# Optimization experiments

Hardware: AMD Instinct MI355X
Metric: run time of the kernel (lower is better)

Reference implementation:

```python
import jax, jax.numpy as jnp
import numpy as np
import math

B, M, N, K = 4, 8192, 8192, 16
FD = 64       # in_fdim == out_fdim (residual add)
HID = 128     # args.hidden_dim
G = 8         # args.ngroups


def index_points(points, idx):
    # points: (B, C, N), idx: (B, M, K) -> (B, C, M, K)
    return jax.vmap(lambda p, i: p[:, i])(points, idx)


def conv1d(x, w, b):  # 1x1 Conv1d: x (B,Ci,M), w (Co,Ci)
    return jnp.einsum('oi,bim->bom', w, x) + b[None, :, None]


def conv2d(x, w, b):  # 1x1 Conv2d: x (B,Ci,M,K), w (Co,Ci)
    return jnp.einsum('oi,bimk->bomk', w, x) + b[None, :, None, None]


def group_norm(x, w, b, eps=1e-5):
    # torch GroupNorm over (C//G, M, K) per group per sample
    Bb, C, Mm, Kk = x.shape
    xr = x.reshape(Bb, G, C // G, Mm, Kk)
    mu = xr.mean(axis=(2, 3, 4), keepdims=True)
    var = xr.var(axis=(2, 3, 4), keepdims=True)
    xr = (xr - mu) * jax.lax.rsqrt(var + eps)
    return xr.reshape(Bb, C, Mm, Kk) * w[None, :, None, None] + b[None, :, None, None]


def setup_inputs() -> dict:
    key = jax.random.key(0)
    ks = jax.random.split(key, 24)
    s = 0.05
    inp = {
        'q_xyzs': jax.random.normal(ks[0], (B, 3, M), jnp.float32),
        'k_xyzs': jax.random.normal(ks[1], (B, 3, N), jnp.float32),
        'q_feats': jax.random.normal(ks[2], (B, FD, M), jnp.float32),
        'k_feats': jax.random.normal(ks[3], (B, FD, N), jnp.float32),
        'v_feats': jax.random.normal(ks[4], (B, FD, N), jnp.float32),
        'knn_idx': jax.random.randint(ks[5], (B, M, K), 0, N),
        'mask': jnp.ones((B, M, K), dtype=bool),
        'wq_w': jax.random.normal(ks[6], (HID, FD)) * s, 'wq_b': jnp.zeros((HID,)),
        'wk_w': jax.random.normal(ks[7], (HID, FD)) * s, 'wk_b': jnp.zeros((HID,)),
        'wv_w': jax.random.normal(ks[8], (HID, FD)) * s, 'wv_b': jnp.zeros((HID,)),
        'd1_w': jax.random.normal(ks[9], (HID, 3)) * s, 'd1_b': jnp.zeros((HID,)),
        'dgn_w': jnp.ones((HID,)), 'dgn_b': jnp.zeros((HID,)),
        'd2_w': jax.random.normal(ks[10], (HID, HID)) * s, 'd2_b': jnp.zeros((HID,)),
        'g1_w': jax.random.normal(ks[11], (HID, HID)) * s, 'g1_b': jnp.zeros((HID,)),
        'ggn_w': jnp.ones((HID,)), 'ggn_b': jnp.zeros((HID,)),
        'g2_w': jax.random.normal(ks[12], (HID, HID)) * s, 'g2_b': jnp.zeros((HID,)),
        'post_w': jax.random.normal(ks[13], (FD, HID)) * s, 'post_b': jnp.zeros((FD,)),
    }
    return inp


def reference(q_xyzs, k_xyzs, q_feats, k_feats, v_feats, knn_idx, mask,
              wq_w, wq_b, wk_w, wk_b, wv_w, wv_b,
              d1_w, d1_b, dgn_w, dgn_b, d2_w, d2_b,
              g1_w, g1_b, ggn_w, ggn_b, g2_w, g2_b,
              post_w, post_b):
    knn_xyzs = index_points(k_xyzs, knn_idx)                 # (B,3,M,K)
    pre = q_feats
    query = conv1d(q_feats, wq_w, wq_b)                      # (B,HID,M)
    key = index_points(conv1d(k_feats, wk_w, wk_b), knn_idx) # (B,HID,M,K)
    value = index_points(conv1d(v_feats, wv_w, wv_b), knn_idx)

    rel = q_xyzs[:, :, :, None] - knn_xyzs                   # (B,3,M,K)
    pos_enc = conv2d(jax.nn.relu(group_norm(conv2d(rel, d1_w, d1_b), dgn_w, dgn_b)), d2_w, d2_b)

    attn_in = query[:, :, :, None] - key + pos_enc
    attn = conv2d(jax.nn.relu(group_norm(conv2d(attn_in, g1_w, g1_b), ggn_w, ggn_b)), g2_w, g2_b)
    attn = attn / math.sqrt(HID)
    attn = jnp.where(mask[:, None], attn, -jnp.finfo(attn.dtype).max)
    attn = jax.nn.softmax(attn, axis=-1)                     # over neighbor axis K

    res = jnp.einsum('bcmk,bcmk->bcm', attn, value + pos_enc)
    return conv1d(res, post_w, post_b) + pre
```

## Files before the change

### kernel.cpp

```cpp
#include <hip/hip_runtime.h>
#include <hip/hip_bf16.h>

typedef __attribute__((ext_vector_type(8))) short short8;
typedef __attribute__((ext_vector_type(4))) float f32x4;
typedef unsigned short ushort_t;

#define B_    4
#define M_    8192
#define N_    8192
#define KNN   16
#define FD    64
#define HID   128
#define CNT   (M_*KNN)
#define SCALE 0.08838834764831845f

#define QT_OFF       0ULL
#define KT_OFF       4194304ULL
#define VT_OFF       6291456ULL
#define WD2_OFF      8388608ULL
#define WFO_OFF      8396800ULL
#define WG2_OFF      8404992ULL
#define WQ2T_OFF     8413184ULL
#define WK2T_OFF     8421376ULL
#define WVT_OFF      8429568ULL
#define POSTT_OFF    8437760ULL
#define G2BS_OFF     8445952ULL
#define BQ_OFF       8446080ULL
#define BK_OFF       8446208ULL
#define HAFF_OFF     8446336ULL
#define RELSTATS_OFF 8448384ULL
#define YSUM_OFF     8448448ULL
#define YSQ_OFF      8448960ULL
#define GGNA_OFF     8449472ULL
#define GGNB_OFF     8449984ULL
#define OUTS_OFF     8450496ULL
#define YW_OFF       10547648ULL
#define VPW_OFF      44102080ULL
#define WS_END_FULL  77656512ULL
#define WS_NEED_FULL (WS_END_FULL * 4ULL)
#define WS_NEED_YW   ((YW_OFF + 33554432ULL) * 4ULL)

__device__ __forceinline__ ushort_t f2bf(float x) {
    return (ushort_t)((__float_as_uint(x) + 0x8000u) >> 16);
}
__device__ __forceinline__ unsigned pk2bf(float a, float b) {
    unsigned ua = __float_as_uint(a) + 0x8000u;
    unsigned ub = __float_as_uint(b) + 0x8000u;
    return (ua >> 16) | (ub & 0xFFFF0000u);
}
__device__ __forceinline__ float bf2f(ushort_t b) {
    union { unsigned u; float f; } v; v.u = ((unsigned)b) << 16;
    return v.f;
}

__global__ __launch_bounds__(256) void k_prep(
    const float* __restrict__ d2, const float* __restrict__ g1, const float* __restrict__ g2,
    const float* __restrict__ wq, const float* __restrict__ wk, const float* __restrict__ wv,
    const float* __restrict__ post, const float* __restrict__ g2b,
    const float* __restrict__ wq_b, const float* __restrict__ wk_b,
    const float* __restrict__ d2b, const float* __restrict__ g1b,
    float* __restrict__ ws)
{
    int tid = blockIdx.x * 256 + threadIdx.x;
    if (tid < 16384) {
        int j = tid & 7, lane = (tid >> 3) & 63, s = (tid >> 9) & 3, ct = tid >> 11;
        int row = ct*16 + (lane & 15);
        int colk = s*32 + (lane >> 4)*8 + j;
        ((ushort_t*)(ws + WD2_OFF))[tid] = f2bf(d2[row*HID + colk]);
        ((ushort_t*)(ws + WG2_OFF))[tid] = f2bf(g2[row*HID + colk] * SCALE);
        float acc = 0.f;
        #pragma unroll 8
        for (int t = 0; t < HID; t++) acc += g1[row*HID + t] * d2[t*HID + colk];
        ((ushort_t*)(ws + WFO_OFF))[tid] = f2bf(acc);
    }
    if (tid < 8192) {
        int f = tid >> 7, j = tid & 127;
        ws[POSTT_OFF + j*64 + f] = post[tid];
        int i = tid >> 7, c = tid & 127;
        float aq = 0.f, ak = 0.f;
        #pragma unroll 8
        for (int h = 0; h < HID; h++) {
            float g = g1[c*HID + h];
            aq += g * wq[h*FD + i];
            ak += g * wk[h*FD + i];
        }
        ws[WQ2T_OFF + tid] = aq;
        ws[WK2T_OFF + tid] = ak;
        ws[WVT_OFF + tid] = wv[c*FD + i];
    }
    if (tid < 128) {
        ws[G2BS_OFF + tid] = g2b[tid] * SCALE;
        float bq = g1b[tid], bk = 0.f;
        #pragma unroll 8
        for (int h = 0; h < HID; h++) {
            float g = g1[tid*HID + h];
            bq += g * (wq_b[h] + d2b[h]);
            bk += g * wk_b[h];
        }
        ws[BQ_OFF + tid] = bq;
        ws[BK_OFF + tid] = bk;
    }
}

__global__ __launch_bounds__(256) void k_transform(
    const float* __restrict__ qf, const float* __restrict__ kf, const float* __restrict__ vf,
    const float* __restrict__ wv_b, float* __restrict__ ws)
{
    __shared__ __align__(16) float sF[64*36];
    int tid = threadIdx.x;
    int t = blockIdx.y;
    int gm0 = blockIdx.x * 32;
    int b = gm0 >> 13, m0 = gm0 & (M_-1);
    const float* in = (t==0) ? qf : (t==1) ? kf : vf;
    const float* wT = ws + ((t==0) ? WQ2T_OFF : (t==1) ? WK2T_OFF : WVT_OFF);
    {
        int i = tid >> 2, sg = tid & 3;
        const float* src = in + ((size_t)b*FD + i)*M_ + m0 + sg*8;
        *(f32x4*)&sF[i*36 + sg*8]     = *(const f32x4*)src;
        *(f32x4*)&sF[i*36 + sg*8 + 4] = *(const f32x4*)(src + 4);
    }
    __syncthreads();
    int c = tid & 127, h = tid >> 7;
    float bc = (t==0) ? ws[BQ_OFF + c] : (t==1) ? ws[BK_OFF + c] : wv_b[c];
    float acc[16];
    #pragma unroll
    for (int p = 0; p < 16; p++) acc[p] = bc;
    #pragma unroll 4
    for (int i = 0; i < 64; i++) {
        float w = wT[i*128 + c];
        #pragma unroll
        for (int pq = 0; pq < 4; pq++) {
            f32x4 fv = *(const f32x4*)&sF[i*36 + h*16 + pq*4];
            acc[pq*4+0] += w*fv[0]; acc[pq*4+1] += w*fv[1];
            acc[pq*4+2] += w*fv[2]; acc[pq*4+3] += w*fv[3];
        }
    }
    if (t == 0) {
        #pragma unroll
        for (int p = 0; p < 16; p++)
            ws[QT_OFF + (size_t)(gm0 + h*16 + p)*HID + c] = acc[p];
    } else {
        ushort_t* o = (ushort_t*)(ws + ((t==1) ? KT_OFF : VT_OFF));
        #pragma unroll
        for (int p = 0; p < 16; p++)
            o[(size_t)(gm0 + h*16 + p)*HID + c] = f2bf(acc[p]);
    }
}

__global__ __launch_bounds__(256) void k_relstats(
    const float* __restrict__ qx, const float* __restrict__ kx,
    const int* __restrict__ knn, float* __restrict__ ws)
{
    int tid = threadIdx.x;
    int b = blockIdx.y;
    int m = blockIdx.x * 256 + tid;
    const float* qb = qx + (size_t)b*3*M_;
    const float* kb = kx + (size_t)b*3*N_;
    const int* kn = knn + ((size_t)b*M_ + m)*KNN;
    float a[9] = {0,0,0,0,0,0,0,0,0};
    float q0 = qb[m], q1 = qb[M_+m], q2 = qb[2*M_+m];
    #pragma unroll
    for (int k = 0; k < KNN; k++) {
        int id = kn[k];
        float r0 = q0 - kb[id], r1 = q1 - kb[N_+id], r2 = q2 - kb[2*N_+id];
        a[0]+=r0; a[1]+=r1; a[2]+=r2;
        a[3]+=r0*r0; a[4]+=r0*r1; a[5]+=r0*r2;
        a[6]+=r1*r1; a[7]+=r1*r2; a[8]+=r2*r2;
    }
    __shared__ float red[4];
    float* rs = ws + RELSTATS_OFF + b*16;
    for (int q = 0; q < 9; q++) {
        float v = a[q];
        #pragma unroll
        for (int o = 32; o > 0; o >>= 1) v += __shfl_down(v, o, 64);
        if ((tid & 63) == 0) red[tid >> 6] = v;
        __syncthreads();
        if (tid == 0) atomicAdd(&rs[q], red[0]+red[1]+red[2]+red[3]);
        __syncthreads();
    }
}

__global__ __launch_bounds__(512) void k_dgn(
    const float* __restrict__ d1w, const float* __restrict__ d1b,
    const float* __restrict__ gw, const float* __restrict__ gb,
    float* __restrict__ ws)
{
    __shared__ float sm_[512], sq_[512], smu[32], srs[32];
    int t = threadIdx.x, b = t >> 7, c = t & 127;
    const float* rs = ws + RELSTATS_OFF + b*16;
    float inv = 1.0f / (float)CNT;
    float x0 = rs[0]*inv, x1 = rs[1]*inv, x2 = rs[2]*inv;
    float S00 = rs[3]*inv, S01 = rs[4]*inv, S02 = rs[5]*inv;
    float S11 = rs[6]*inv, S12 = rs[7]*inv, S22 = rs[8]*inv;
    float w0 = d1w[c*3], w1 = d1w[c*3+1], w2 = d1w[c*3+2], bc = d1b[c];
    float mc = w0*x0 + w1*x1 + w2*x2 + bc;
    float qc = w0*w0*S00 + w1*w1*S11 + w2*w2*S22
             + 2.f*(w0*w1*S01 + w0*w2*S02 + w1*w2*S12)
             + 2.f*bc*(mc - bc) + bc*bc;
    sm_[t] = mc; sq_[t] = qc;
    __syncthreads();
    if (t < 32) {
        int bb = t >> 3, g = t & 7;
        float mu = 0, ey = 0;
        for (int j = 0; j < 16; j++) { mu += sm_[bb*128 + g*16 + j]; ey += sq_[bb*128 + g*16 + j]; }
        mu *= (1.f/16.f); ey *= (1.f/16.f);
        smu[t] = mu; srs[t] = rsqrtf(ey - mu*mu + 1e-5f);
    }
    __syncthreads();
    int g = c >> 4;
    float al = gw[c] * srs[b*8 + g];
    float be = gb[c] - smu[b*8 + g] * al;
    f32x4 h; h[0] = al*w0; h[1] = al*w1; h[2] = al*w2; h[3] = al*bc + be;
    *(f32x4*)(ws + HAFF_OFF + ((size_t)b*128 + c)*4) = h;
}

__global__ __launch_bounds__(512) void k_ggn(
    const float* __restrict__ gw, const float* __restrict__ gb, float* __restrict__ ws)
{
    __shared__ float smu[32], srs[32];
    int t = threadIdx.x, b = t >> 7, c = t & 127;
    if (t < 32) {
        int bb = t >> 3, g = t & 7;
        float s1 = 0, s2 = 0;
        for (int j = 0; j < 16; j++) {
            s1 += ws[YSUM_OFF + bb*128 + g*16 + j];
            s2 += ws[YSQ_OFF  + bb*128 + g*16 + j];
        }
        float invn = 1.f / (16.f * (float)CNT);
        float mu = s1*invn, ey = s2*invn;
        smu[t] = mu; srs[t] = rsqrtf(ey - mu*mu + 1e-5f);
    }
    __syncthreads();
    int g = c >> 4;
    float al = gw[c] * srs[b*8 + g];
    float be = gb[c] - smu[b*8 + g] * al;
    ws[GGNA_OFF + b*128 + c] = al;
    ws[GGNB_OFF + b*128 + c] = be;
}

struct SmemStats {
    f32x4 haff[128];
    float rel[4][16][4];
    ushort_t tH[4][16*136];
    float ga[128], gb[128];
    int idx[64];
};

__global__ __launch_bounds__(256, 4) void k_statsbig(
    const float* __restrict__ qx, const float* __restrict__ kx, const int* __restrict__ knn,
    const float* __restrict__ d2b, float* __restrict__ ws)
{
    __shared__ SmemStats sm;
    int tid = threadIdx.x, wid = tid >> 6, lane = tid & 63;
    int ln = lane & 15, q = lane >> 4;
    int gm0 = blockIdx.x * 4;
    int b = gm0 >> 13, m0 = gm0 & (M_-1);
    int ct0 = wid * 2;

    if (tid < 64) {
        int id = knn[(size_t)gm0*KNN + tid];
        sm.idx[tid] = id;
        int p = tid >> 4, nn = tid & 15;
        int m = m0 + p;
        sm.rel[p][nn][0] = qx[(size_t)b*3*M_ + m]        - kx[(size_t)b*3*N_ + id];
        sm.rel[p][nn][1] = qx[(size_t)b*3*M_ + M_ + m]   - kx[(size_t)b*3*N_ + N_ + id];
        sm.rel[p][nn][2] = qx[(size_t)b*3*M_ + 2*M_ + m] - kx[(size_t)b*3*N_ + 2*N_ + id];
    }
    if (tid < 128) {
        sm.haff[tid] = *(const f32x4*)(ws + HAFF_OFF + ((size_t)b*128 + tid)*4);
        sm.ga[tid] = 0.f; sm.gb[tid] = 0.f;
    }
    __syncthreads();

    const ushort_t* ktb = (const ushort_t*)(ws + KT_OFF);
    const ushort_t* vtb = (const ushort_t*)(ws + VT_OFF);

    uint2 kvp[4][2], vvp[4][2];
    #pragma unroll
    for (int p = 0; p < 4; p++) {
        int id = sm.idx[p*16 + ln];
        const ushort_t* kr = ktb + ((size_t)b*N_ + id)*HID;
        const ushort_t* vr = vtb + ((size_t)b*N_ + id)*HID;
        #pragma unroll
        for (int cc = 0; cc < 2; cc++) {
            kvp[p][cc] = *(const uint2*)(kr + (ct0+cc)*16 + q*4);
            vvp[p][cc] = *(const uint2*)(vr + (ct0+cc)*16 + q*4);
        }
    }

    {
        int p = tid >> 6, n = (tid >> 2) & 15, cb = tid & 3;
        float r0 = sm.rel[p][n][0];
        float r1 = sm.rel[p][n][1];
        float r2 = sm.rel[p][n][2];
        unsigned* dst = (unsigned*)&sm.tH[p][n*136 + cb*32];
        int rot = ((((n >> 3) & 1) | (((cb >> 1) & 1) << 1)) << 2);
        #pragma unroll
        for (int t = 0; t < 16; t++) {
            int o = (t + rot) & 15;
            f32x4 h1 = sm.haff[cb*32 + 2*o];
            f32x4 h2 = sm.haff[cb*32 + 2*o + 1];
            float a = fmaf(h1[0], r0, fmaf(h1[1], r1, fmaf(h1[2], r2, h1[3])));
            float c = fmaf(h2[0], r0, fmaf(h2[1], r1, fmaf(h2[2], r2, h2[3])));
            dst[o] = pk2bf(a > 0.f ? a : 0.f, c > 0.f ? c : 0.f);
        }
    }
    __syncthreads();

    const short8* wfo = (const short8*)(ws + WFO_OFF);
    const short8* wd2 = (const short8*)(ws + WD2_OFF);
    uint2* yw8 = (uint2*)(ws + YW_OFF);
    uint2* vp8 = (uint2*)(ws + VPW_OFF);

    float s1[2][4], s2[2][4];
    #pragma unroll
    for (int cc = 0; cc < 2; cc++)
        #pragma unroll
        for (int r = 0; r < 4; r++) { s1[cc][r] = 0.f; s2[cc][r] = 0.f; }

    #pragma unroll
    for (int p = 0; p < 4; p++) {
        int gm = gm0 + p;
        short8 bh[4];
        #pragma unroll
        for (int s = 0; s < 4; s++)
            bh[s] = *(const short8*)&sm.tH[p][ln*136 + s*32 + q*8];

        #pragma unroll
        for (int cc = 0; cc < 2; cc++) {
            f32x4 a = {0.f,0.f,0.f,0.f};
            #pragma unroll
            for (int s = 0; s < 4; s++)
                a = __builtin_amdgcn_mfma_f32_16x16x32_bf16(wd2[((ct0+cc)*4+s)*64 + lane], bh[s], a, 0,0,0);
            int row0 = (ct0+cc)*16 + q*4;
            f32x4 bi = *(const f32x4*)(d2b + row0);
            uint2 vv = vvp[p][cc];
            uint2 pv;
            pv.x = pk2bf(a[0]+bi[0]+bf2f((ushort_t)(vv.x & 0xffff)),
                         a[1]+bi[1]+bf2f((ushort_t)(vv.x >> 16)));
            pv.y = pk2bf(a[2]+bi[2]+bf2f((ushort_t)(vv.y & 0xffff)),
                         a[3]+bi[3]+bf2f((ushort_t)(vv.y >> 16)));
            vp8[((size_t)gm*8 + ct0+cc)*64 + lane] = pv;
        }
        #pragma unroll
        for (int cc = 0; cc < 2; cc++) {
            f32x4 a = {0.f,0.f,0.f,0.f};
            #pragma unroll
            for (int s = 0; s < 4; s++)
                a = __builtin_amdgcn_mfma_f32_16x16x32_bf16(wfo[((ct0+cc)*4+s)*64 + lane], bh[s], a, 0,0,0);
            int row0 = (ct0+cc)*16 + q*4;
            f32x4 qv = *(const f32x4*)(ws + QT_OFF + (size_t)gm*HID + row0);
            uint2 kv = kvp[p][cc];
            float y0 = a[0] + qv[0] - bf2f((ushort_t)(kv.x & 0xffff));
            float y1 = a[1] + qv[1] - bf2f((ushort_t)(kv.x >> 16));
            float y2 = a[2] + qv[2] - bf2f((ushort_t)(kv.y & 0xffff));
            float y3 = a[3] + qv[3] - bf2f((ushort_t)(kv.y >> 16));
            s1[cc][0]+=y0; s1[cc][1]+=y1; s1[cc][2]+=y2; s1[cc][3]+=y3;
            s2[cc][0]+=y0*y0; s2[cc][1]+=y1*y1; s2[cc][2]+=y2*y2; s2[cc][3]+=y3*y3;
            uint2 yv; yv.x = pk2bf(y0,y1); yv.y = pk2bf(y2,y3);
            yw8[((size_t)gm*8 + ct0+cc)*64 + lane] = yv;
        }
    }

    #pragma unroll
    for (int cc = 0; cc < 2; cc++)
        #pragma unroll
        for (int r = 0; r < 4; r++) {
            float v1 = s1[cc][r], v2 = s2[cc][r];
            v1 += __shfl_xor(v1,1,64); v1 += __shfl_xor(v1,2,64);
            v1 += __shfl_xor(v1,4,64); v1 += __shfl_xor(v1,8,64);
            v2 += __shfl_xor(v2,1,64); v2 += __shfl_xor(v2,2,64);
            v2 += __shfl_xor(v2,4,64); v2 += __shfl_xor(v2,8,64);
            if (ln == 0) {
                atomicAdd(&sm.ga[(ct0+cc)*16 + q*4 + r], v1);
                atomicAdd(&sm.gb[(ct0+cc)*16 + q*4 + r], v2);
            }
        }
    __syncthreads();
    if (tid < 128) {
        atomicAdd(&ws[YSUM_OFF + b*128 + tid], sm.ga[tid]);
        atomicAdd(&ws[YSQ_OFF  + b*128 + tid], sm.gb[tid]);
    }
}

struct SmemFinal {
    ushort_t tY[4][16*136];
    ushort_t tVP[4][16*136];
    float ga[128], gb[128];
    float res[4][128];
};

__global__ __launch_bounds__(256, 4) void k_final(
    const float* __restrict__ postb, float* __restrict__ ws)
{
    __shared__ SmemFinal sm;
    int tid = threadIdx.x, wid = tid >> 6, lane = tid & 63;
    int ln = lane & 15, q = lane >> 4;
    int gm0 = blockIdx.x * 4;
    int b = gm0 >> 13;
    int ct0 = wid * 2;

    if (tid < 128) {
        sm.ga[tid] = ws[GGNA_OFF + b*128 + tid];
        sm.gb[tid] = ws[GGNB_OFF + b*128 + tid];
    }
    __syncthreads();

    const uint2* yw8 = (const uint2*)(ws + YW_OFF);
    const uint2* vp8 = (const uint2*)(ws + VPW_OFF);

    #pragma unroll
    for (int p = 0; p < 4; p++) {
        int gm = gm0 + p;
        #pragma unroll
        for (int cc = 0; cc < 2; cc++) {
            int ct = ct0 + cc, row0 = ct*16 + q*4;
            uint2 yv = yw8[((size_t)gm*8 + ct)*64 + lane];
            f32x4 ga = *(const f32x4*)&sm.ga[row0];
            f32x4 gb = *(const f32x4*)&sm.gb[row0];
            float t0 = fmaf(ga[0], bf2f((ushort_t)(yv.x & 0xffff)), gb[0]);
            float t1 = fmaf(ga[1], bf2f((ushort_t)(yv.x >> 16)),    gb[1]);
            float t2 = fmaf(ga[2], bf2f((ushort_t)(yv.y & 0xffff)), gb[2]);
            float t3 = fmaf(ga[3], bf2f((ushort_t)(yv.y >> 16)),    gb[3]);
            uint2 yq2;
            yq2.x = pk2bf(t0 > 0.f ? t0 : 0.f, t1 > 0.f ? t1 : 0.f);
            yq2.y = pk2bf(t2 > 0.f ? t2 : 0.f, t3 > 0.f ? t3 : 0.f);
            *(uint2*)&sm.tY[p][ln*136 + row0] = yq2;
            *(uint2*)&sm.tVP[p][ln*136 + row0] = vp8[((size_t)gm*8 + ct)*64 + lane];
        }
    }
    __syncthreads();

    {
        const short8* wg2 = (const short8*)(ws + WG2_OFF);
        #pragma unroll
        for (int p = 0; p < 4; p++) {
            short8 ay[4];
            #pragma unroll
            for (int s = 0; s < 4; s++)
                ay[s] = *(const short8*)&sm.tY[p][ln*136 + s*32 + q*8];
            #pragma unroll
            for (int cc = 0; cc < 2; cc++) {
                int cout = (ct0+cc)*16 + ln;
                f32x4 a = {0.f,0.f,0.f,0.f};
                #pragma unroll
                for (int s = 0; s < 4; s++)
                    a = __builtin_amdgcn_mfma_f32_16x16x32_bf16(ay[s], wg2[((ct0+cc)*4+s)*64 + lane], a, 0,0,0);
                float zb = ws[G2BS_OFF + cout];
                float den = 0.f, num = 0.f;
                #pragma unroll
                for (int r = 0; r < 4; r++) {
                    float e = __expf(a[r] + zb);
                    den += e;
                    num += e * bf2f(sm.tVP[p][(q*4+r)*136 + cout]);
                }
                den += __shfl_xor(den, 16, 64); den += __shfl_xor(den, 32, 64);
                num += __shfl_xor(num, 16, 64); num += __shfl_xor(num, 32, 64);
                if (q == 0) sm.res[p][cout] = num / den;
            }
        }
    }
    __syncthreads();

    {
        int f = tid >> 2, p = tid & 3;
        const float* pt = ws + POSTT_OFF;
        const float* rr = sm.res[p];
        float acc = postb[f];
        #pragma unroll 8
        for (int j = 0; j < 128; j++) acc += pt[j*64 + f] * rr[j];
        ws[OUTS_OFF + (size_t)(gm0 + p)*FD + f] = acc;
    }
}

struct SmemPipe {
    union {
        ushort_t tP[4][16*136];
        struct { f32x4 haff[128]; float rel[4][16][4]; } pre;
    } u;
    ushort_t tH[4][16*136];
    float ga[128], gb[128];
    float res[4][128];
    int idx[64];
};

template<bool STATS, bool STOREY, bool LOADY>
__global__ __launch_bounds__(256, 4) void k_pipe(
    const float* __restrict__ qx, const float* __restrict__ kx, const int* __restrict__ knn,
    const float* __restrict__ d2b, const float* __restrict__ postb,
    float* __restrict__ ws)
{
    __shared__ SmemPipe sm;
    int tid = threadIdx.x, wid = tid >> 6, lane = tid & 63;
    int ln = lane & 15, q = lane >> 4;
    int gm0 = blockIdx.x * 4;
    int b = gm0 >> 13, m0 = gm0 & (M_-1);
    int ct0 = wid * 2;

    if (tid < 64) {
        int id = knn[(size_t)gm0*KNN + tid];
        sm.idx[tid] = id;
        int p = tid >> 4, nn = tid & 15;
        int m = m0 + p;
        sm.u.pre.rel[p][nn][0] = qx[(size_t)b*3*M_ + m]        - kx[(size_t)b*3*N_ + id];
        sm.u.pre.rel[p][nn][1] = qx[(size_t)b*3*M_ + M_ + m]   - kx[(size_t)b*3*N_ + N_ + id];
        sm.u.pre.rel[p][nn][2] = qx[(size_t)b*3*M_ + 2*M_ + m] - kx[(size_t)b*3*N_ + 2*N_ + id];
    }
    if (tid < 128) {
        sm.u.pre.haff[tid] = *(const f32x4*)(ws + HAFF_OFF + ((size_t)b*128 + tid)*4);
        if (STATS) { sm.ga[tid] = 0.f; sm.gb[tid] = 0.f; }
        else { sm.ga[tid] = ws[GGNA_OFF + b*128 + tid]; sm.gb[tid] = ws[GGNB_OFF + b*128 + tid]; }
    }
    __syncthreads();

    const ushort_t* ktb = (const ushort_t*)(ws + KT_OFF);
    const ushort_t* vtb = (const ushort_t*)(ws + VT_OFF);

    uint2 kvp[4][2];
    if (!LOADY) {
        #pragma unroll
        for (int p = 0; p < 4; p++) {
            int id = sm.idx[p*16 + ln];
            const ushort_t* kr = ktb + ((size_t)b*N_ + id)*HID;
            #pragma unroll
            for (int cc = 0; cc < 2; cc++)
                kvp[p][cc] = *(const uint2*)(kr + (ct0+cc)*16 + q*4);
        }
    }

    {
        int p = tid >> 6, n = (tid >> 2) & 15, cb = tid & 3;
        float r0 = sm.u.pre.rel[p][n][0];
        float r1 = sm.u.pre.rel[p][n][1];
        float r2 = sm.u.pre.rel[p][n][2];
        unsigned* dst = (unsigned*)&sm.tH[p][n*136 + cb*32];
        int rot = ((((n >> 3) & 1) | (((cb >> 1) & 1) << 1)) << 2);
        #pragma unroll
        for (int t = 0; t < 16; t++) {
            int o = (t + rot) & 15;
            f32x4 h1 = sm.u.pre.haff[cb*32 + 2*o];
            f32x4 h2 = sm.u.pre.haff[cb*32 + 2*o + 1];
            float a = fmaf(h1[0], r0, fmaf(h1[1], r1, fmaf(h1[2], r2, h1[3])));
            float c = fmaf(h2[0], r0, fmaf(h2[1], r1, fmaf(h2[2], r2, h2[3])));
            dst[o] = pk2bf(a > 0.f ? a : 0.f, c > 0.f ? c : 0.f);
        }
    }
    __syncthreads();

    const short8* wfo = (const short8*)(ws + WFO_OFF);
    const short8* wd2 = (const short8*)(ws + WD2_OFF);

    float s1[2][4], s2[2][4];
    if (STATS) {
        #pragma unroll
        for (int cc = 0; cc < 2; cc++)
            #pragma unroll
            for (int r = 0; r < 4; r++) { s1[cc][r] = 0.f; s2[cc][r] = 0.f; }
    }
    uint2 yp[4][2];
    f32x4 bid2[2], ga_[2], gb_[2];
    #pragma unroll
    for (int cc = 0; cc < 2; cc++) {
        int row0 = (ct0+cc)*16 + q*4;
        if (!STATS) {
            bid2[cc] = *(const f32x4*)(d2b + row0);
            ga_[cc] = *(const f32x4*)&sm.ga[row0];
            gb_[cc] = *(const f32x4*)&sm.gb[row0];
        }
    }

    #pragma unroll
    for (int p = 0; p < 4; p++) {
        int gm = gm0 + p;
        short8 bh[4];
        #pragma unroll
        for (int s = 0; s < 4; s++)
            bh[s] = *(const short8*)&sm.tH[p][ln*136 + s*32 + q*8];

        if (!LOADY) {
            #pragma unroll
            for (int cc = 0; cc < 2; cc++) {
                int row0 = (ct0+cc)*16 + q*4;
                f32x4 a = {0.f,0.f,0.f,0.f};
                #pragma unroll
                for (int s = 0; s < 4; s++)
                    a = __builtin_amdgcn_mfma_f32_16x16x32_bf16(wfo[((ct0+cc)*4+s)*64 + lane], bh[s], a, 0,0,0);
                f32x4 qv = *(const f32x4*)(ws + QT_OFF + (size_t)gm*HID + row0);
                uint2 kv = kvp[p][cc];
                float y0 = a[0] + qv[0] - bf2f((ushort_t)(kv.x & 0xffff));
                float y1 = a[1] + qv[1] - bf2f((ushort_t)(kv.x >> 16));
                float y2 = a[2] + qv[2] - bf2f((ushort_t)(kv.y & 0xffff));
                float y3 = a[3] + qv[3] - bf2f((ushort_t)(kv.y >> 16));
                if (STATS) {
                    s1[cc][0]+=y0; s1[cc][1]+=y1; s1[cc][2]+=y2; s1[cc][3]+=y3;
                    s2[cc][0]+=y0*y0; s2[cc][1]+=y1*y1; s2[cc][2]+=y2*y2; s2[cc][3]+=y3*y3;
                    if (STOREY) { yp[p][cc].x = pk2bf(y0,y1); yp[p][cc].y = pk2bf(y2,y3); }
                } else {
                    float t0 = fmaf(ga_[cc][0], y0, gb_[cc][0]);
                    float t1 = fmaf(ga_[cc][1], y1, gb_[cc][1]);
                    float t2 = fmaf(ga_[cc][2], y2, gb_[cc][2]);
                    float t3 = fmaf(ga_[cc][3], y3, gb_[cc][3]);
                    yp[p][cc].x = pk2bf(t0 > 0.f ? t0 : 0.f, t1 > 0.f ? t1 : 0.f);
                    yp[p][cc].y = pk2bf(t2 > 0.f ? t2 : 0.f, t3 > 0.f ? t3 : 0.f);
                }
            }
        }
        if (!STATS) {
            #pragma unroll
            for (int cc = 0; cc < 2; cc++) {
                f32x4 a = {0.f,0.f,0.f,0.f};
                #pragma unroll
                for (int s = 0; s < 4; s++)
                    a = __builtin_amdgcn_mfma_f32_16x16x32_bf16(wd2[((ct0+cc)*4+s)*64 + lane], bh[s], a, 0,0,0);
                int row0 = (ct0+cc)*16 + q*4;
                uint2 pv;
                pv.x = pk2bf(a[0]+bid2[cc][0], a[1]+bid2[cc][1]);
                pv.y = pk2bf(a[2]+bid2[cc][2], a[3]+bid2[cc][3]);
                *(uint2*)&sm.u.tP[p][ln*136 + row0] = pv;
            }
        }
    }

    if (STATS) {
        if (STOREY) {
            __syncthreads();
            #pragma unroll
            for (int p = 0; p < 4; p++)
                #pragma unroll
                for (int cc = 0; cc < 2; cc++)
                    *(uint2*)&sm.tH[p][ln*136 + (ct0+cc)*16 + q*4] = yp[p][cc];
            __syncthreads();
            {
                int p = tid >> 6, n = (tid >> 2) & 15, cb = tid & 3;
                ushort_t* yw = (ushort_t*)(ws + YW_OFF);
                const short8* src = (const short8*)&sm.tH[p][n*136 + cb*32];
                short8* dst = (short8*)(yw + ((size_t)(gm0+p)*16 + n)*HID + cb*32);
                #pragma unroll
                for (int u = 0; u < 4; u++) dst[u] = src[u];
            }
        }
        #pragma unroll
        for (int cc = 0; cc < 2; cc++)
            #pragma unroll
            for (int r = 0; r < 4; r++) {
                float v1 = s1[cc][r], v2 = s2[cc][r];
                v1 += __shfl_xor(v1,1,64); v1 += __shfl_xor(v1,2,64);
                v1 += __shfl_xor(v1,4,64); v1 += __shfl_xor(v1,8,64);
                v2 += __shfl_xor(v2,1,64); v2 += __shfl_xor(v2,2,64);
                v2 += __shfl_xor(v2,4,64); v2 += __shfl_xor(v2,8,64);
                if (ln == 0) {
                    atomicAdd(&sm.ga[(ct0+cc)*16 + q*4 + r], v1);
                    atomicAdd(&sm.gb[(ct0+cc)*16 + q*4 + r], v2);
                }
            }
        __syncthreads();
        if (tid < 128) {
            atomicAdd(&ws[YSUM_OFF + b*128 + tid], sm.ga[tid]);
            atomicAdd(&ws[YSQ_OFF  + b*128 + tid], sm.gb[tid]);
        }
        return;
    }

    __syncthreads();

    if (LOADY) {
        int p = tid >> 6, n = (tid >> 2) & 15, cb = tid & 3;
        const ushort_t* yw = (const ushort_t*)(ws + YW_OFF);
        const short8* src = (const short8*)(yw + ((size_t)(gm0+p)*16 + n)*HID + cb*32);
        ushort_t* dst = &sm.tH[p][n*136 + cb*32];
        #pragma unroll
        for (int u = 0; u < 4; u++) {
            short8 yv8 = src[u];
            unsigned w[4];
            #pragma unroll
            for (int j = 0; j < 4; j++) {
                float ga0 = sm.ga[cb*32 + u*8 + j*2],   gb0 = sm.gb[cb*32 + u*8 + j*2];
                float ga1 = sm.ga[cb*32 + u*8 + j*2+1], gb1 = sm.gb[cb*32 + u*8 + j*2+1];
                float ya = fmaf(ga0, bf2f((ushort_t)yv8[j*2]),   gb0);
                float yb = fmaf(ga1, bf2f((ushort_t)yv8[j*2+1]), gb1);
                w[j] = pk2bf(ya > 0.f ? ya : 0.f, yb > 0.f ? yb : 0.f);
            }
            *(short8*)(dst + u*8) = *(short8*)w;
        }
    } else {
        #pragma unroll
        for (int p = 0; p < 4; p++)
            #pragma unroll
            for (int cc = 0; cc < 2; cc++)
                *(uint2*)&sm.tH[p][ln*136 + (ct0+cc)*16 + q*4] = yp[p][cc];
    }
    {
        int p = tid >> 6, n = (tid >> 2) & 15, cb = tid & 3;
        int id = sm.idx[p*16 + n];
        const ushort_t* vr = vtb + ((size_t)b*N_ + id)*HID + cb*32;
        ushort_t* pr = &sm.u.tP[p][n*136 + cb*32];
        #pragma unroll
        for (int u = 0; u < 4; u++) {
            short8 vv = *(const short8*)(vr + u*8);
            short8 pp = *(const short8*)(pr + u*8);
            unsigned w[4];
            #pragma unroll
            for (int j = 0; j < 4; j++) {
                float a = bf2f((ushort_t)vv[j*2])   + bf2f((ushort_t)pp[j*2]);
                float c = bf2f((ushort_t)vv[j*2+1]) + bf2f((ushort_t)pp[j*2+1]);
                w[j] = pk2bf(a, c);
            }
            *(short8*)(pr + u*8) = *(short8*)w;
        }
    }
    __syncthreads();

    {
        const short8* wg2 = (const short8*)(ws + WG2_OFF);
        #pragma unroll
        for (int p = 0; p < 4; p++) {
            short8 ay[4];
            #pragma unroll
            for (int s = 0; s < 4; s++)
                ay[s] = *(const short8*)&sm.tH[p][ln*136 + s*32 + q*8];
            #pragma unroll
            for (int cc = 0; cc < 2; cc++) {
                int cout = (ct0+cc)*16 + ln;
                f32x4 a = {0.f,0.f,0.f,0.f};
                #pragma unroll
                for (int s = 0; s < 4; s++)
                    a = __builtin_amdgcn_mfma_f32_16x16x32_bf16(ay[s], wg2[((ct0+cc)*4+s)*64 + lane], a, 0,0,0);
                float zb = ws[G2BS_OFF + cout];
                float den = 0.f, num = 0.f;
                #pragma unroll
                for (int r = 0; r < 4; r++) {
                    float e = __expf(a[r] + zb);
                    den += e;
                    num += e * bf2f(sm.u.tP[p][(q*4+r)*136 + cout]);
                }
                den += __shfl_xor(den, 16, 64); den += __shfl_xor(den, 32, 64);
                num += __shfl_xor(num, 16, 64); num += __shfl_xor(num, 32, 64);
                if (q == 0) sm.res[p][cout] = num / den;
            }
        }
    }
    __syncthreads();

    {
        int f = tid >> 2, p = tid & 3;
        const float* pt = ws + POSTT_OFF;
        const float* rr = sm.res[p];
        float acc = postb[f];
        #pragma unroll 8
        for (int j = 0; j < 128; j++) acc += pt[j*64 + f] * rr[j];
        ws[OUTS_OFF + (size_t)(gm0 + p)*FD + f] = acc;
    }
}

__global__ __launch_bounds__(256) void k_out(
    const float* __restrict__ qf, const float* __restrict__ ws, float* __restrict__ out)
{
    __shared__ float sT[64][65];
    int tid = threadIdx.x;
    int b = blockIdx.y, m0 = blockIdx.x * 64;
    const float* stg = ws + OUTS_OFF + ((size_t)b*M_ + m0)*FD;
    #pragma unroll
    for (int it = 0; it < 16; it++) {
        int idx = it*256 + tid;
        sT[idx >> 6][idx & 63] = stg[idx];
    }
    __syncthreads();
    #pragma unroll
    for (int it = 0; it < 16; it++) {
        int idx = it*256 + tid;
        int f = idx >> 6, mm = idx & 63;
        size_t o = (size_t)b*FD*M_ + (size_t)f*M_ + m0 + mm;
        out[o] = sT[mm][f] + qf[o];
    }
}

extern "C" void kernel_launch(void* const* d_in, const int* in_sizes, int n_in,
                              void* d_out, int out_size, void* d_ws, size_t ws_size,
                              hipStream_t stream)
{
    const float* q_xyzs = (const float*)d_in[0];
    const float* k_xyzs = (const float*)d_in[1];
    const float* q_feats= (const float*)d_in[2];
    const float* k_feats= (const float*)d_in[3];
    const float* v_feats= (const float*)d_in[4];
    const int*   knn    = (const int*)d_in[5];
    const float* wq_w = (const float*)d_in[7];  const float* wq_b = (const float*)d_in[8];
    const float* wk_w = (const float*)d_in[9];  const float* wk_b = (const float*)d_in[10];
    const float* wv_w = (const float*)d_in[11]; const float* wv_b = (const float*)d_in[12];
    const float* d1_w = (const float*)d_in[13]; const float* d1_b = (const float*)d_in[14];
    const float* dgn_w= (const float*)d_in[15]; const float* dgn_b= (const float*)d_in[16];
    const float* d2_w = (const float*)d_in[17]; const float* d2_b = (const float*)d_in[18];
    const float* g1_w = (const float*)d_in[19]; const float* g1_b = (const float*)d_in[20];
    const float* ggn_w= (const float*)d_in[21]; const float* ggn_b= (const float*)d_in[22];
    const float* g2_w = (const float*)d_in[23]; const float* g2_b = (const float*)d_in[24];
    const float* post_w=(const float*)d_in[25]; const float* post_b=(const float*)d_in[26];
    float* ws  = (float*)d_ws;
    float* out = (float*)d_out;

    bool full = (ws_size >= WS_NEED_FULL);
    bool yw   = (ws_size >= WS_NEED_YW);

    hipMemsetAsync(ws + RELSTATS_OFF, 0, 1088*sizeof(float), stream);

    k_prep<<<64, 256, 0, stream>>>(d2_w, g1_w, g2_w, wq_w, wk_w, wv_w,
                                   post_w, g2_b, wq_b, wk_b, d2_b, g1_b, ws);
    k_transform<<<dim3(B_*M_/32, 3), 256, 0, stream>>>(q_feats, k_feats, v_feats, wv_b, ws);
    k_relstats<<<dim3(M_/256, B_), 256, 0, stream>>>(q_xyzs, k_xyzs, knn, ws);
    k_dgn<<<1, 512, 0, stream>>>(d1_w, d1_b, dgn_w, dgn_b, ws);
    if (full) {
        k_statsbig<<<B_*M_/4, 256, 0, stream>>>(q_xyzs, k_xyzs, knn, d2_b, ws);
        k_ggn<<<1, 512, 0, stream>>>(ggn_w, ggn_b, ws);
        k_final<<<B_*M_/4, 256, 0, stream>>>(post_b, ws);
    } else if (yw) {
        k_pipe<true, true, false><<<B_*M_/4, 256, 0, stream>>>(q_xyzs, k_xyzs, knn, d2_b, post_b, ws);
        k_ggn<<<1, 512, 0, stream>>>(ggn_w, ggn_b, ws);
        k_pipe<false, false, true><<<B_*M_/4, 256, 0, stream>>>(q_xyzs, k_xyzs, knn, d2_b, post_b, ws);
    } else {
        k_pipe<true, false, false><<<B_*M_/4, 256, 0, stream>>>(q_xyzs, k_xyzs, knn, d2_b, post_b, ws);
        k_ggn<<<1, 512, 0, stream>>>(ggn_w, ggn_b, ws);
        k_pipe<false, false, false><<<B_*M_/4, 256, 0, stream>>>(q_xyzs, k_xyzs, knn, d2_b, post_b, ws);
    }
    k_out<<<dim3(M_/64, B_), 256, 0, stream>>>(q_feats, ws, out);
}
```

Measured before the change: 489.6 us.

## Store pre-norm activations as fp8, Q as bf16, fuse output residual into final kernels

The pre-GroupNorm activation buffer is now written as packed fp8 instead of bf16, and the query projection is stored as bf16 instead of fp32. This halves the intermediate traffic and shrinks the workspace. The separate k_out transpose kernel is removed, and the final kernels write the residual-added output straight to the output tensor. The Y layout in k_pipe is switched to the lane-native fragment order, and Y/VP loads are prefetched into registers early. Fp8 quantisation of pre-norm values adds precision risk, and the direct output stores are strided by M, which may be poorly coalesced.

```diff
diff --git a/kernel.cpp b/kernel.cpp
--- a/kernel.cpp
+++ b/kernel.cpp
@@ -3,6 +3,7 @@
 
 typedef __attribute__((ext_vector_type(8))) short short8;
 typedef __attribute__((ext_vector_type(4))) float f32x4;
+typedef __attribute__((ext_vector_type(2))) float f32x2;
 typedef unsigned short ushort_t;
 
 #define B_    4
@@ -15,29 +16,27 @@
 #define SCALE 0.08838834764831845f
 
 #define QT_OFF       0ULL
-#define KT_OFF       4194304ULL
-#define VT_OFF       6291456ULL
-#define WD2_OFF      8388608ULL
-#define WFO_OFF      8396800ULL
-#define WG2_OFF      8404992ULL
-#define WQ2T_OFF     8413184ULL
-#define WK2T_OFF     8421376ULL
-#define WVT_OFF      8429568ULL
-#define POSTT_OFF    8437760ULL
-#define G2BS_OFF     8445952ULL
-#define BQ_OFF       8446080ULL
-#define BK_OFF       8446208ULL
-#define HAFF_OFF     8446336ULL
-#define RELSTATS_OFF 8448384ULL
-#define YSUM_OFF     8448448ULL
-#define YSQ_OFF      8448960ULL
-#define GGNA_OFF     8449472ULL
-#define GGNB_OFF     8449984ULL
-#define OUTS_OFF     8450496ULL
-#define YW_OFF       10547648ULL
-#define VPW_OFF      44102080ULL
-#define WS_END_FULL  77656512ULL
-#define WS_NEED_FULL (WS_END_FULL * 4ULL)
+#define KT_OFF       2097152ULL
+#define VT_OFF       4194304ULL
+#define WD2_OFF      6291456ULL
+#define WFO_OFF      6299648ULL
+#define WG2_OFF      6307840ULL
+#define WQ2T_OFF     6316032ULL
+#define WK2T_OFF     6324224ULL
+#define WVT_OFF      6332416ULL
+#define POSTT_OFF    6340608ULL
+#define G2BS_OFF     6348800ULL
+#define BQ_OFF       6348928ULL
+#define BK_OFF       6349056ULL
+#define HAFF_OFF     6349184ULL
+#define RELSTATS_OFF 6351232ULL
+#define YSUM_OFF     6351296ULL
+#define YSQ_OFF      6351808ULL
+#define GGNA_OFF     6352320ULL
+#define GGNB_OFF     6352832ULL
+#define YW_OFF       6353344ULL
+#define VPW_OFF      23130560ULL
+#define WS_NEED_F8   (56684992ULL * 4ULL)
 #define WS_NEED_YW   ((YW_OFF + 33554432ULL) * 4ULL)
 
 __device__ __forceinline__ ushort_t f2bf(float x) {
@@ -51,6 +50,11 @@
 __device__ __forceinline__ float bf2f(ushort_t b) {
     union { unsigned u; float f; } v; v.u = ((unsigned)b) << 16;
     return v.f;
+}
+__device__ __forceinline__ unsigned pk4fp8(float a, float b, float c, float d) {
+    int v = __builtin_amdgcn_cvt_pk_fp8_f32(a, b, 0, false);
+    v = __builtin_amdgcn_cvt_pk_fp8_f32(c, d, v, true);
+    return (unsigned)v;
 }
 
 __global__ __launch_bounds__(256) void k_prep(
@@ -135,16 +139,10 @@
             acc[pq*4+2] += w*fv[2]; acc[pq*4+3] += w*fv[3];
         }
     }
-    if (t == 0) {
-        #pragma unroll
-        for (int p = 0; p < 16; p++)
-            ws[QT_OFF + (size_t)(gm0 + h*16 + p)*HID + c] = acc[p];
-    } else {
-        ushort_t* o = (ushort_t*)(ws + ((t==1) ? KT_OFF : VT_OFF));
-        #pragma unroll
-        for (int p = 0; p < 16; p++)
-            o[(size_t)(gm0 + h*16 + p)*HID + c] = f2bf(acc[p]);
-    }
+    ushort_t* o = (ushort_t*)(ws + ((t==0) ? QT_OFF : (t==1) ? KT_OFF : VT_OFF));
+    #pragma unroll
+    for (int p = 0; p < 16; p++)
+        o[(size_t)(gm0 + h*16 + p)*HID + c] = f2bf(acc[p]);
 }
 
 __global__ __launch_bounds__(256) void k_relstats(
@@ -272,6 +270,7 @@
     }
     __syncthreads();
 
+    const ushort_t* qtb = (const ushort_t*)(ws + QT_OFF);
     const ushort_t* ktb = (const ushort_t*)(ws + KT_OFF);
     const ushort_t* vtb = (const ushort_t*)(ws + VT_OFF);
 
@@ -309,7 +308,7 @@
 
     const short8* wfo = (const short8*)(ws + WFO_OFF);
     const short8* wd2 = (const short8*)(ws + WD2_OFF);
-    uint2* yw8 = (uint2*)(ws + YW_OFF);
+    unsigned* yf8 = (unsigned*)(ws + YW_OFF);
     uint2* vp8 = (uint2*)(ws + VPW_OFF);
 
     float s1[2][4], s2[2][4];
@@ -349,16 +348,15 @@
             for (int s = 0; s < 4; s++)
                 a = __builtin_amdgcn_mfma_f32_16x16x32_bf16(wfo[((ct0+cc)*4+s)*64 + lane], bh[s], a, 0,0,0);
             int row0 = (ct0+cc)*16 + q*4;
-            f32x4 qv = *(const f32x4*)(ws + QT_OFF + (size_t)gm*HID + row0);
+            uint2 qv = *(const uint2*)(qtb + (size_t)gm*HID + row0);
             uint2 kv = kvp[p][cc];
-            float y0 = a[0] + qv[0] - bf2f((ushort_t)(kv.x & 0xffff));
-            float y1 = a[1] + qv[1] - bf2f((ushort_t)(kv.x >> 16));
-            float y2 = a[2] + qv[2] - bf2f((ushort_t)(kv.y & 0xffff));
-            float y3 = a[3] + qv[3] - bf2f((ushort_t)(kv.y >> 16));
+            float y0 = a[0] + bf2f((ushort_t)(qv.x & 0xffff)) - bf2f((ushort_t)(kv.x & 0xffff));
+            float y1 = a[1] + bf2f((ushort_t)(qv.x >> 16))    - bf2f((ushort_t)(kv.x >> 16));
+            float y2 = a[2] + bf2f((ushort_t)(qv.y & 0xffff)) - bf2f((ushort_t)(kv.y & 0xffff));
+            float y3 = a[3] + bf2f((ushort_t)(qv.y >> 16))    - bf2f((ushort_t)(kv.y >> 16));
             s1[cc][0]+=y0; s1[cc][1]+=y1; s1[cc][2]+=y2; s1[cc][3]+=y3;
             s2[cc][0]+=y0*y0; s2[cc][1]+=y1*y1; s2[cc][2]+=y2*y2; s2[cc][3]+=y3*y3;
-            uint2 yv; yv.x = pk2bf(y0,y1); yv.y = pk2bf(y2,y3);
-            yw8[((size_t)gm*8 + ct0+cc)*64 + lane] = yv;
+            yf8[((size_t)gm*8 + ct0+cc)*64 + lane] = pk4fp8(y0, y1, y2, y3);
         }
     }
 
@@ -391,14 +389,26 @@
 };
 
 __global__ __launch_bounds__(256, 4) void k_final(
-    const float* __restrict__ postb, float* __restrict__ ws)
+    const float* __restrict__ postb, const float* __restrict__ qf,
+    float* __restrict__ ws, float* __restrict__ out)
 {
     __shared__ SmemFinal sm;
     int tid = threadIdx.x, wid = tid >> 6, lane = tid & 63;
     int ln = lane & 15, q = lane >> 4;
     int gm0 = blockIdx.x * 4;
-    int b = gm0 >> 13;
+    int b = gm0 >> 13, m0 = gm0 & (M_-1);
     int ct0 = wid * 2;
+
+    const unsigned* yf8 = (const unsigned*)(ws + YW_OFF);
+    const uint2* vp8 = (const uint2*)(ws + VPW_OFF);
+    unsigned yv_[4][2]; uint2 vp_[4][2];
+    #pragma unroll
+    for (int p = 0; p < 4; p++)
+        #pragma unroll
+        for (int cc = 0; cc < 2; cc++) {
+            yv_[p][cc] = yf8[((size_t)(gm0+p)*8 + ct0+cc)*64 + lane];
+            vp_[p][cc] = vp8[((size_t)(gm0+p)*8 + ct0+cc)*64 + lane];
+        }
 
     if (tid < 128) {
         sm.ga[tid] = ws[GGNA_OFF + b*128 + tid];
@@ -406,29 +416,25 @@
     }
     __syncthreads();
 
-    const uint2* yw8 = (const uint2*)(ws + YW_OFF);
-    const uint2* vp8 = (const uint2*)(ws + VPW_OFF);
-
-    #pragma unroll
-    for (int p = 0; p < 4; p++) {
-        int gm = gm0 + p;
+    #pragma unroll
+    for (int p = 0; p < 4; p++)
         #pragma unroll
         for (int cc = 0; cc < 2; cc++) {
-            int ct = ct0 + cc, row0 = ct*16 + q*4;
-            uint2 yv = yw8[((size_t)gm*8 + ct)*64 + lane];
+            int row0 = (ct0+cc)*16 + q*4;
+            f32x2 lo = __builtin_amdgcn_cvt_pk_f32_fp8((int)yv_[p][cc], false);
+            f32x2 hi = __builtin_amdgcn_cvt_pk_f32_fp8((int)yv_[p][cc], true);
             f32x4 ga = *(const f32x4*)&sm.ga[row0];
             f32x4 gb = *(const f32x4*)&sm.gb[row0];
-            float t0 = fmaf(ga[0], bf2f((ushort_t)(yv.x & 0xffff)), gb[0]);
-            float t1 = fmaf(ga[1], bf2f((ushort_t)(yv.x >> 16)),    gb[1]);
-            float t2 = fmaf(ga[2], bf2f((ushort_t)(yv.y & 0xffff)), gb[2]);
-            float t3 = fmaf(ga[3], bf2f((ushort_t)(yv.y >> 16)),    gb[3]);
+            float t0 = fmaf(ga[0], lo[0], gb[0]);
+            float t1 = fmaf(ga[1], lo[1], gb[1]);
+            float t2 = fmaf(ga[2], hi[0], gb[2]);
+            float t3 = fmaf(ga[3], hi[1], gb[3]);
             uint2 yq2;
             yq2.x = pk2bf(t0 > 0.f ? t0 : 0.f, t1 > 0.f ? t1 : 0.f);
             yq2.y = pk2bf(t2 > 0.f ? t2 : 0.f, t3 > 0.f ? t3 : 0.f);
             *(uint2*)&sm.tY[p][ln*136 + row0] = yq2;
-            *(uint2*)&sm.tVP[p][ln*136 + row0] = vp8[((size_t)gm*8 + ct)*64 + lane];
-        }
-    }
+            *(uint2*)&sm.tVP[p][ln*136 + row0] = vp_[p][cc];
+        }
     __syncthreads();
 
     {
@@ -469,7 +475,8 @@
         float acc = postb[f];
         #pragma unroll 8
         for (int j = 0; j < 128; j++) acc += pt[j*64 + f] * rr[j];
-        ws[OUTS_OFF + (size_t)(gm0 + p)*FD + f] = acc;
+        size_t o = (size_t)b*FD*M_ + (size_t)f*M_ + m0 + p;
+        out[o] = acc + qf[o];
     }
 }
 
@@ -488,7 +495,7 @@
 __global__ __launch_bounds__(256, 4) void k_pipe(
     const float* __restrict__ qx, const float* __restrict__ kx, const int* __restrict__ knn,
     const float* __restrict__ d2b, const float* __restrict__ postb,
-    float* __restrict__ ws)
+    const float* __restrict__ qf, float* __restrict__ ws, float* __restrict__ out)
 {
     __shared__ SmemPipe sm;
     int tid = threadIdx.x, wid = tid >> 6, lane = tid & 63;
@@ -496,6 +503,16 @@
     int gm0 = blockIdx.x * 4;
     int b = gm0 >> 13, m0 = gm0 & (M_-1);
     int ct0 = wid * 2;
+
+    uint2 ywp[4][2];
+    if (LOADY) {
+        const uint2* yw8 = (const uint2*)(ws + YW_OFF);
+        #pragma unroll
+        for (int p = 0; p < 4; p++)
+            #pragma unroll
+            for (int cc = 0; cc < 2; cc++)
+                ywp[p][cc] = yw8[((size_t)(gm0+p)*8 + ct0+cc)*64 + lane];
+    }
 
     if (tid < 64) {
         int id = knn[(size_t)gm0*KNN + tid];
@@ -513,6 +530,7 @@
     }
     __syncthreads();
 
+    const ushort_t* qtb = (const ushort_t*)(ws + QT_OFF);
     const ushort_t* ktb = (const ushort_t*)(ws + KT_OFF);
     const ushort_t* vtb = (const ushort_t*)(ws + VT_OFF);
 
@@ -585,12 +603,12 @@
                 #pragma unroll
                 for (int s = 0; s < 4; s++)
                     a = __builtin_amdgcn_mfma_f32_16x16x32_bf16(wfo[((ct0+cc)*4+s)*64 + lane], bh[s], a, 0,0,0);
-                f32x4 qv = *(const f32x4*)(ws + QT_OFF + (size_t)gm*HID + row0);
+                uint2 qv = *(const uint2*)(qtb + (size_t)gm*HID + row0);
                 uint2 kv = kvp[p][cc];
-                float y0 = a[0] + qv[0] - bf2f((ushort_t)(kv.x & 0xffff));
-                float y1 = a[1] + qv[1] - bf2f((ushort_t)(kv.x >> 16));
-                float y2 = a[2] + qv[2] - bf2f((ushort_t)(kv.y & 0xffff));
-                float y3 = a[3] + qv[3] - bf2f((ushort_t)(kv.y >> 16));
+                float y0 = a[0] + bf2f((ushort_t)(qv.x & 0xffff)) - bf2f((ushort_t)(kv.x & 0xffff));
+                float y1 = a[1] + bf2f((ushort_t)(qv.x >> 16))    - bf2f((ushort_t)(kv.x >> 16));
+                float y2 = a[2] + bf2f((ushort_t)(qv.y & 0xffff)) - bf2f((ushort_t)(kv.y & 0xffff));
+                float y3 = a[3] + bf2f((ushort_t)(qv.y >> 16))    - bf2f((ushort_t)(kv.y >> 16));
                 if (STATS) {
                     s1[cc][0]+=y0; s1[cc][1]+=y1; s1[cc][2]+=y2; s1[cc][3]+=y3;
                     s2[cc][0]+=y0*y0; s2[cc][1]+=y1*y1; s2[cc][2]+=y2*y2; s2[cc][3]+=y3*y3;
@@ -623,21 +641,12 @@
 
     if (STATS) {
         if (STOREY) {
-            __syncthreads();
+            uint2* yw8 = (uint2*)(ws + YW_OFF);
             #pragma unroll
             for (int p = 0; p < 4; p++)
                 #pragma unroll
                 for (int cc = 0; cc < 2; cc++)
-                    *(uint2*)&sm.tH[p][ln*136 + (ct0+cc)*16 + q*4] = yp[p][cc];
-            __syncthreads();
-            {
-                int p = tid >> 6, n = (tid >> 2) & 15, cb = tid & 3;
-                ushort_t* yw = (ushort_t*)(ws + YW_OFF);
-                const short8* src = (const short8*)&sm.tH[p][n*136 + cb*32];
-                short8* dst = (short8*)(yw + ((size_t)(gm0+p)*16 + n)*HID + cb*32);
-                #pragma unroll
-                for (int u = 0; u < 4; u++) dst[u] = src[u];
-            }
+                    yw8[((size_t)(gm0+p)*8 + ct0+cc)*64 + lane] = yp[p][cc];
         }
         #pragma unroll
         for (int cc = 0; cc < 2; cc++)
@@ -664,24 +673,21 @@
     __syncthreads();
 
     if (LOADY) {
-        int p = tid >> 6, n = (tid >> 2) & 15, cb = tid & 3;
-        const ushort_t* yw = (const ushort_t*)(ws + YW_OFF);
-        const short8* src = (const short8*)(yw + ((size_t)(gm0+p)*16 + n)*HID + cb*32);
-        ushort_t* dst = &sm.tH[p][n*136 + cb*32];
-        #pragma unroll
-        for (int u = 0; u < 4; u++) {
-            short8 yv8 = src[u];
-            unsigned w[4];
-            #pragma unroll
-            for (int j = 0; j < 4; j++) {
-                float ga0 = sm.ga[cb*32 + u*8 + j*2],   gb0 = sm.gb[cb*32 + u*8 + j*2];
-                float ga1 = sm.ga[cb*32 + u*8 + j*2+1], gb1 = sm.gb[cb*32 + u*8 + j*2+1];
-                float ya = fmaf(ga0, bf2f((ushort_t)yv8[j*2]),   gb0);
-                float yb = fmaf(ga1, bf2f((ushort_t)yv8[j*2+1]), gb1);
-                w[j] = pk2bf(ya > 0.f ? ya : 0.f, yb > 0.f ? yb : 0.f);
+        #pragma unroll
+        for (int p = 0; p < 4; p++)
+            #pragma unroll
+            for (int cc = 0; cc < 2; cc++) {
+                int row0 = (ct0+cc)*16 + q*4;
+                uint2 yv = ywp[p][cc];
+                float t0 = fmaf(ga_[cc][0], bf2f((ushort_t)(yv.x & 0xffff)), gb_[cc][0]);
+                float t1 = fmaf(ga_[cc][1], bf2f((ushort_t)(yv.x >> 16)),    gb_[cc][1]);
+                float t2 = fmaf(ga_[cc][2], bf2f((ushort_t)(yv.y & 0xffff)), gb_[cc][2]);
+                float t3 = fmaf(ga_[cc][3], bf2f((ushort_t)(yv.y >> 16)),    gb_[cc][3]);
+                uint2 yq2;
+                yq2.x = pk2bf(t0 > 0.f ? t0 : 0.f, t1 > 0.f ? t1 : 0.f);
+                yq2.y = pk2bf(t2 > 0.f ? t2 : 0.f, t3 > 0.f ? t3 : 0.f);
+                *(uint2*)&sm.tH[p][ln*136 + row0] = yq2;
             }
-            *(short8*)(dst + u*8) = *(short8*)w;
-        }
     } else {
         #pragma unroll
         for (int p = 0; p < 4; p++)
@@ -748,29 +754,8 @@
         float acc = postb[f];
         #pragma unroll 8
         for (int j = 0; j < 128; j++) acc += pt[j*64 + f] * rr[j];
-        ws[OUTS_OFF + (size_t)(gm0 + p)*FD + f] = acc;
-    }
-}
-
-__global__ __launch_bounds__(256) void k_out(
-    const float* __restrict__ qf, const float* __restrict__ ws, float* __restrict__ out)
-{
-    __shared__ float sT[64][65];
-    int tid = threadIdx.x;
-    int b = blockIdx.y, m0 = blockIdx.x * 64;
-    const float* stg = ws + OUTS_OFF + ((size_t)b*M_ + m0)*FD;
-    #pragma unroll
-    for (int it = 0; it < 16; it++) {
-        int idx = it*256 + tid;
-        sT[idx >> 6][idx & 63] = stg[idx];
-    }
-    __syncthreads();
-    #pragma unroll
-    for (int it = 0; it < 16; it++) {
-        int idx = it*256 + tid;
-        int f = idx >> 6, mm = idx & 63;
-        size_t o = (size_t)b*FD*M_ + (size_t)f*M_ + m0 + mm;
-        out[o] = sT[mm][f] + qf[o];
+        size_t o = (size_t)b*FD*M_ + (size_t)f*M_ + m0 + p;
+        out[o] = acc + qf[o];
     }
 }
 
@@ -797,8 +782,8 @@
     float* ws  = (float*)d_ws;
     float* out = (float*)d_out;
 
-    bool full = (ws_size >= WS_NEED_FULL);
-    bool yw   = (ws_size >= WS_NEED_YW);
+    bool f8 = (ws_size >= WS_NEED_F8);
+    bool yw = (ws_size >= WS_NEED_YW);
 
     hipMemsetAsync(ws + RELSTATS_OFF, 0, 1088*sizeof(float), stream);
 
@@ -807,18 +792,17 @@
     k_transform<<<dim3(B_*M_/32, 3), 256, 0, stream>>>(q_feats, k_feats, v_feats, wv_b, ws);
     k_relstats<<<dim3(M_/256, B_), 256, 0, stream>>>(q_xyzs, k_xyzs, knn, ws);
     k_dgn<<<1, 512, 0, stream>>>(d1_w, d1_b, dgn_w, dgn_b, ws);
-    if (full) {
+    if (f8) {
         k_statsbig<<<B_*M_/4, 256, 0, stream>>>(q_xyzs, k_xyzs, knn, d2_b, ws);
         k_ggn<<<1, 512, 0, stream>>>(ggn_w, ggn_b, ws);
-        k_final<<<B_*M_/4, 256, 0, stream>>>(post_b, ws);
+        k_final<<<B_*M_/4, 256, 0, stream>>>(post_b, q_feats, ws, out);
     } else if (yw) {
-        k_pipe<true, true, false><<<B_*M_/4, 256, 0, stream>>>(q_xyzs, k_xyzs, knn, d2_b, post_b, ws);
+        k_pipe<true, true, false><<<B_*M_/4, 256, 0, stream>>>(q_xyzs, k_xyzs, knn, d2_b, post_b, q_feats, ws, out);
         k_ggn<<<1, 512, 0, stream>>>(ggn_w, ggn_b, ws);
-        k_pipe<false, false, true><<<B_*M_/4, 256, 0, stream>>>(q_xyzs, k_xyzs, knn, d2_b, post_b, ws);
+        k_pipe<false, false, true><<<B_*M_/4, 256, 0, stream>>>(q_xyzs, k_xyzs, knn, d2_b, post_b, q_feats, ws, out);
     } else {
-        k_pipe<true, false, false><<<B_*M_/4, 256, 0, stream>>>(q_xyzs, k_xyzs, knn, d2_b, post_b, ws);
+        k_pipe<true, false, false><<<B_*M_/4, 256, 0, stream>>>(q_xyzs, k_xyzs, knn, d2_b, post_b, q_feats, ws, out);
         k_ggn<<<1, 512, 0, stream>>>(ggn_w, ggn_b, ws);
-        k_pipe<false, false, false><<<B_*M_/4, 256, 0, stream>>>(q_xyzs, k_xyzs, knn, d2_b, post_b, ws);
-    }
-    k_out<<<dim3(M_/64, B_), 256, 0, stream>>>(q_feats, ws, out);
-}
+        k_pipe<false, false, false><<<B_*M_/4, 256, 0, stream>>>(q_xyzs, k_xyzs, knn, d2_b, post_b, q_feats, ws, out);
+    }
+}
```

Result: slower. 557.8 us (+13.9%).
